# Kernel optimization log

Hardware: AMD Instinct MI355X
Metric: run time of the kernel (lower is better)

Reference implementation:

```python
import jax, jax.numpy as jnp
import numpy as np

OUT_STEPS = 32
UNITS = 512
FEATURES = 64


def setup_inputs() -> dict:
    key = jax.random.key(0)
    ks = jax.random.split(key, 4)
    B, T, F, U = 2048, 128, FEATURES, UNITS
    scale = 0.05
    return {
        "inputs": jax.random.normal(ks[0], (B, T, F), dtype=jnp.float32),
        "W_x": jax.random.normal(ks[1], (F, 4 * U), dtype=jnp.float32) * scale,
        "W_h": jax.random.normal(ks[2], (U, 4 * U), dtype=jnp.float32) * scale,
        "b": jnp.zeros((4 * U,), dtype=jnp.float32),
        "dense_W": jax.random.normal(ks[3], (U, F), dtype=jnp.float32) * scale,
        "dense_b": jnp.zeros((F,), dtype=jnp.float32),
    }


def reference(inputs, W_x, W_h, b, dense_W, dense_b):
    U = W_h.shape[0]
    B = inputs.shape[0]

    def cell(h, c, x):
        # Keras LSTMCell: gates in i, f, g(c), o order
        z = x @ W_x + h @ W_h + b  # [B, 4U]
        i, f, g, o = jnp.split(z, 4, axis=-1)
        i = jax.nn.sigmoid(i)
        f = jax.nn.sigmoid(f)
        g = jnp.tanh(g)
        o = jax.nn.sigmoid(o)
        c2 = f * c + i * g
        h2 = o * jnp.tanh(c2)
        return h2, c2

    h0 = jnp.zeros((B, U), inputs.dtype)
    c0 = jnp.zeros((B, U), inputs.dtype)

    def warm_step(carry, x_t):
        h, c = carry
        h, c = cell(h, c, x_t)
        return (h, c), None

    (h, c), _ = jax.lax.scan(warm_step, (h0, c0), jnp.swapaxes(inputs, 0, 1))
    pred = h @ dense_W + dense_b  # [B, F]

    def dec_step(carry, _):
        p, hh, cc = carry
        hh, cc = cell(hh, cc, p)
        p2 = hh @ dense_W + dense_b
        return (p2, hh, cc), p2

    _, rest = jax.lax.scan(dec_step, (pred, h, c), None, length=OUT_STEPS - 1)
    preds = jnp.concatenate([pred[None], rest], axis=0)  # [out_steps, B, F]
    return jnp.swapaxes(preds, 0, 1)  # [B, out_steps, F]
```

## Files before the change

### kernel.cpp

```cpp
#include <hip/hip_runtime.h>
#include <hip/hip_bf16.h>

#define B_ 2048
#define T_ 128
#define F_ 64
#define U_ 512
#define FOURU 2048
#define OUTS 32
#define ROWS 128
#define COLSB 128
#define KTOT 576
#define LDSTR 584

typedef __attribute__((ext_vector_type(8))) short bf16x8;
typedef __attribute__((ext_vector_type(4))) float f32x4;

#define OFF_CNT   0
#define OFF_HBUF  69632
#define OFF_WT    (OFF_HBUF + 2*B_*U_*2)
#define OFF_WDEC  (OFF_WT + FOURU*KTOT*2)
#define OFF_DWT   (OFF_WDEC + FOURU*U_*2)
#define OFF_BDEC  (OFF_DWT + F_*U_*2)
#define OFF_XBF   (OFF_BDEC + FOURU*4)
#define WS_TOTAL  (OFF_XBF + (size_t)T_*B_*F_*2)

__device__ __forceinline__ short f2bf(float f) {
  union { float f; unsigned u; } a; a.f = f;
  unsigned u = a.u;
  unsigned r = u + 0x7FFFu + ((u >> 16) & 1u);
  return (short)(r >> 16);
}
__device__ __forceinline__ float sigm(float x){ return 1.0f/(1.0f+__expf(-x)); }
__device__ __forceinline__ float tanh_(float x){ return 1.0f - 2.0f/(1.0f+__expf(2.0f*x)); }

__global__ void prep_wt(const float* __restrict__ Wx, const float* __restrict__ Wh,
                        short* __restrict__ Wt) {
  int idx = blockIdx.x*256 + threadIdx.x;
  if (idx >= FOURU*KTOT) return;
  int c = idx / KTOT, k = idx % KTOT;
  float v = (k < F_) ? Wx[(size_t)k*FOURU + c] : Wh[(size_t)(k-F_)*FOURU + c];
  Wt[idx] = f2bf(v);
}
__global__ void prep_wdec(const float* __restrict__ Wh, const float* __restrict__ Wx,
                          const float* __restrict__ Dw, short* __restrict__ Wdec) {
  int idx = blockIdx.x*256 + threadIdx.x;
  if (idx >= FOURU*U_) return;
  int c = idx / U_, u = idx % U_;
  float a = Wh[(size_t)u*FOURU + c];
  for (int f=0; f<F_; ++f) a += Dw[u*F_ + f] * Wx[(size_t)f*FOURU + c];
  Wdec[idx] = f2bf(a);
}
__global__ void prep_bdec(const float* __restrict__ bv, const float* __restrict__ db,
                          const float* __restrict__ Wx, float* __restrict__ bdec) {
  int c = blockIdx.x*256 + threadIdx.x;
  if (c >= FOURU) return;
  float a = bv[c];
  for (int f=0; f<F_; ++f) a += db[f]*Wx[(size_t)f*FOURU + c];
  bdec[c] = a;
}
__global__ void prep_dwt(const float* __restrict__ Dw, short* __restrict__ Dwt) {
  int idx = blockIdx.x*256 + threadIdx.x;
  if (idx >= F_*U_) return;
  int f = idx / U_, u = idx % U_;
  Dwt[idx] = f2bf(Dw[u*F_ + f]);
}
__global__ void prep_x(const float* __restrict__ in, short* __restrict__ xbf) {
  int idx = blockIdx.x*256 + threadIdx.x;
  if (idx >= T_*B_*F_) return;
  int f = idx % F_, b = (idx / F_) % B_, t = idx / (F_*B_);
  xbf[idx] = f2bf(in[((size_t)b*T_ + t)*F_ + f]);
}

__global__ __launch_bounds__(1024, 4) void lstm_main(
    const short* __restrict__ xbf, const short* __restrict__ Wt,
    const short* __restrict__ Wdec, const short* __restrict__ Dwt,
    const float* __restrict__ bvec, const float* __restrict__ bdec,
    const float* __restrict__ dbv, short* hbuf, unsigned* cnt,
    float* __restrict__ out)
{
  __shared__ short wlds[COLSB*LDSTR];
  __shared__ int sSame;
  const int tid = threadIdx.x;
  const int bidx = blockIdx.x;
  const int gb = (bidx & 7)*2 + (bidx >> 7);
  const int gu = (bidx >> 3) & 15;

  unsigned* flags  = cnt + gb*1024;
  unsigned* myFlag = flags + gu*64;
  unsigned* regCnt = cnt + 16384 + gb*16;
  unsigned* xcdTab = cnt + 16640 + gb*16;

  {
    unsigned xcc;
    asm volatile("s_getreg_b32 %0, hwreg(HW_REG_XCC_ID)" : "=s"(xcc));
    if (tid == 0) {
      __hip_atomic_store(&xcdTab[gu], xcc + 1u, __ATOMIC_RELAXED, __HIP_MEMORY_SCOPE_AGENT);
      __hip_atomic_fetch_add(regCnt, 1u, __ATOMIC_RELEASE, __HIP_MEMORY_SCOPE_AGENT);
      while (__hip_atomic_fetch_add(regCnt, 0u, __ATOMIC_RELAXED, __HIP_MEMORY_SCOPE_AGENT) < 16u)
        __builtin_amdgcn_s_sleep(2);
      __builtin_amdgcn_fence(__ATOMIC_ACQUIRE, "agent");
      unsigned x0 = __hip_atomic_load(&xcdTab[0], __ATOMIC_RELAXED, __HIP_MEMORY_SCOPE_AGENT);
      int same = 1;
      for (int i = 1; i < 16; ++i)
        same &= (__hip_atomic_load(&xcdTab[i], __ATOMIC_RELAXED, __HIP_MEMORY_SCOPE_AGENT) == x0);
      sSame = same;
    }
  }

  {
    const int c = tid >> 3, q = tid & 7;
    const int gate = (c >> 4) & 3;
    const int u = gu*32 + ((c >> 6) << 4) + (c & 15);
    const int gcol = gate*512 + u;
    const short* src = Wt + (size_t)gcol*KTOT + q*72;
    short* dst = wlds + c*LDSTR + q*72;
    #pragma unroll
    for (int j=0;j<9;j++)
      *(bf16x8*)(dst + j*8) = *(const bf16x8*)(src + j*8);
  }
  __syncthreads();
  const bool fastSync = (sSame != 0);

  const int w = tid >> 6, lane = tid & 63;
  const int wm = w >> 1, wn = w & 1;
  const int l15 = lane & 15, kh = lane >> 4;

  const int ucol = gu*32 + wn*16 + l15;
  float bia[4], biaD[4];
  #pragma unroll
  for (int g=0; g<4; ++g){ bia[g] = bvec[g*512 + ucol]; biaD[g] = bdec[g*512 + ucol]; }

  float cst[4] = {};
  const int rowA = gb*ROWS + wm*16 + l15;

  bf16x8 Bc[2][4];
  auto loadBc = [&]() {
    #pragma unroll
    for (int ks=0; ks<2; ++ks)
      #pragma unroll
      for (int g=0; g<4; ++g)
        Bc[ks][g] = *(const bf16x8*)(wlds + (size_t)(wn*64 + 16*g + l15)*LDSTR + 64 + ks*32 + kh*8);
  };
  loadBc();

  f32x4 acc[4];
  auto do_x = [&](int tt) {
    const short* xp = xbf + ((size_t)tt*B_ + rowA)*F_ + kh*8;
    bf16x8 a0 = *(const bf16x8*)(xp);
    bf16x8 a1 = *(const bf16x8*)(xp + 32);
    #pragma unroll
    for (int g=0; g<4; ++g) {
      bf16x8 b0 = *(const bf16x8*)(wlds + (size_t)(wn*64 + 16*g + l15)*LDSTR + kh*8);
      bf16x8 b1 = *(const bf16x8*)(wlds + (size_t)(wn*64 + 16*g + l15)*LDSTR + 32 + kh*8);
      f32x4 z = {0.f,0.f,0.f,0.f};
      z = __builtin_amdgcn_mfma_f32_16x16x32_bf16(a0, b0, z, 0,0,0);
      acc[g] = __builtin_amdgcn_mfma_f32_16x16x32_bf16(a1, b1, z, 0,0,0);
    }
  };
  do_x(0);

  for (int t = 0; t < 160; ++t) {
    if (t > 0) {
      if (fastSync) {
        if (tid < 64) {
          unsigned* fl = flags + (tid & 15)*64;
          const bool poller = (tid < 16);
          for (;;) {
            unsigned vv = poller
              ? __hip_atomic_load(fl, __ATOMIC_RELAXED, __HIP_MEMORY_SCOPE_AGENT)
              : (unsigned)t;
            if (__ballot(vv >= (unsigned)t) == ~0ull) break;
            __builtin_amdgcn_s_sleep(2);
          }
          asm volatile("buffer_inv sc0" ::: "memory");
          asm volatile("s_waitcnt vmcnt(0)" ::: "memory");
        }
      } else {
        if (tid < 64) {
          unsigned* fl = flags + (tid & 15)*64;
          const bool poller = (tid < 16);
          for (;;) {
            unsigned vv = poller
              ? __hip_atomic_fetch_add(fl, 0u, __ATOMIC_RELAXED, __HIP_MEMORY_SCOPE_AGENT)
              : (unsigned)t;
            if (__ballot(vv >= (unsigned)t) == ~0ull) break;
            __builtin_amdgcn_s_sleep(2);
          }
        }
        if (tid == 0)
          __builtin_amdgcn_fence(__ATOMIC_ACQUIRE, "agent");
      }
      __syncthreads();
    }

    const short* hcur = hbuf + (size_t)(t & 1)*B_*U_;
    short* hnxt = hbuf + (size_t)((t+1) & 1)*B_*U_;

    if (t >= 128 && gu < 8 && w < 4) {
      const int s = t - 128;
      const int pr0 = gb*ROWS + gu*16 + l15;
      f32x4 pa = {0.f,0.f,0.f,0.f};
      #pragma unroll
      for (int ks=0; ks<16; ++ks) {
        bf16x8 a = *(const bf16x8*)(hcur + (size_t)pr0*U_ + ks*32 + kh*8);
        bf16x8 b = *(const bf16x8*)(Dwt + (size_t)(w*16 + l15)*U_ + ks*32 + kh*8);
        pa = __builtin_amdgcn_mfma_f32_16x16x32_bf16(a, b, pa, 0,0,0);
      }
      const int col = w*16 + l15;
      const float dbc = dbv[col];
      #pragma unroll
      for (int r=0; r<4; ++r) {
        const int orow = gb*ROWS + gu*16 + kh*4 + r;
        out[((size_t)orow*OUTS + s)*F_ + col] = pa[r] + dbc;
      }
    }
    if (t == 159) break;
    if (t == 128) {
      __syncthreads();
      const int c = tid >> 3, q = tid & 7;
      const int gate = (c >> 4) & 3;
      const int u = gu*32 + ((c >> 6) << 4) + (c & 15);
      const int gcol = gate*512 + u;
      const short* src = Wdec + (size_t)gcol*U_ + q*64;
      short* dst = wlds + c*LDSTR + 64 + q*64;
      #pragma unroll
      for (int j=0;j<8;j++)
        *(bf16x8*)(dst + j*8) = *(const bf16x8*)(src + j*8);
      __syncthreads();
      loadBc();
    }

    {
      const short* hp = hcur + (size_t)rowA*U_ + kh*8;
      #pragma unroll
      for (int ks=0; ks<16; ++ks) {
        bf16x8 a = *(const bf16x8*)(hp + ks*32);
        #pragma unroll
        for (int g=0; g<4; ++g) {
          bf16x8 b = (ks < 2) ? Bc[ks][g]
            : *(const bf16x8*)(wlds + (size_t)(wn*64 + 16*g + l15)*LDSTR + 64 + ks*32 + kh*8);
          acc[g] = __builtin_amdgcn_mfma_f32_16x16x32_bf16(a, b, acc[g], 0,0,0);
        }
      }
    }

    {
      const bool warm = (t < T_);
      #pragma unroll
      for (int r=0; r<4; ++r) {
        float zi = acc[0][r] + (warm ? bia[0] : biaD[0]);
        float zf = acc[1][r] + (warm ? bia[1] : biaD[1]);
        float zg = acc[2][r] + (warm ? bia[2] : biaD[2]);
        float zo = acc[3][r] + (warm ? bia[3] : biaD[3]);
        float ig = sigm(zi), fg = sigm(zf), gg = tanh_(zg), og = sigm(zo);
        float c2 = fmaf(fg, cst[r], ig*gg);
        cst[r] = c2;
        float h2 = og*tanh_(c2);
        const int row = gb*ROWS + wm*16 + kh*4 + r;
        hnxt[(size_t)row*U_ + ucol] = f2bf(h2);
      }
    }

    __syncthreads();
    if (tid == 0) {
      if (fastSync)
        __hip_atomic_store(myFlag, (unsigned)(t+1), __ATOMIC_RELAXED, __HIP_MEMORY_SCOPE_AGENT);
      else
        __hip_atomic_fetch_add(myFlag, 1u, __ATOMIC_RELEASE, __HIP_MEMORY_SCOPE_AGENT);
    }

    #pragma unroll
    for (int g=0; g<4; ++g) acc[g] = (f32x4){0.f,0.f,0.f,0.f};
    if (t + 1 < T_) do_x(t+1);
  }
}

extern "C" void kernel_launch(void* const* d_in, const int* in_sizes, int n_in,
                              void* d_out, int out_size, void* d_ws, size_t ws_size,
                              hipStream_t stream) {
  const float* inputs = (const float*)d_in[0];
  const float* Wx = (const float*)d_in[1];
  const float* Wh = (const float*)d_in[2];
  const float* bv = (const float*)d_in[3];
  const float* Dw = (const float*)d_in[4];
  const float* db = (const float*)d_in[5];
  float* out = (float*)d_out;
  char* ws = (char*)d_ws;
  if (ws_size < WS_TOTAL) return;

  unsigned* cnt = (unsigned*)(ws + OFF_CNT);
  short* hbuf = (short*)(ws + OFF_HBUF);
  short* Wt   = (short*)(ws + OFF_WT);
  short* Wdec = (short*)(ws + OFF_WDEC);
  short* Dwt  = (short*)(ws + OFF_DWT);
  float* bdec = (float*)(ws + OFF_BDEC);
  short* xbf  = (short*)(ws + OFF_XBF);

  hipMemsetAsync(d_ws, 0, OFF_HBUF + (size_t)B_*U_*2, stream);
  prep_wt  <<<(FOURU*KTOT+255)/256, 256, 0, stream>>>(Wx, Wh, Wt);
  prep_wdec<<<(FOURU*U_ +255)/256, 256, 0, stream>>>(Wh, Wx, Dw, Wdec);
  prep_bdec<<<(FOURU     +255)/256, 256, 0, stream>>>(bv, db, Wx, bdec);
  prep_dwt <<<(F_*U_     +255)/256, 256, 0, stream>>>(Dw, Dwt);
  prep_x   <<<(T_*B_*F_  +255)/256, 256, 0, stream>>>(inputs, xbf);
  lstm_main<<<256, 1024, 0, stream>>>(xbf, Wt, Wdec, Dwt, bv, bdec, db, hbuf, cnt, out);
}
```

Before: 1.851 ms.

## Replace block-level barrier sync with per-wave flag counting and move dense head after publish

Each wave now polls the inter-block flags itself and bumps a shared counter after its own h stores. This replaces the block-wide __syncthreads and single-thread flag write, so waves no longer wait on the slowest wave in their block at each timestep. The dense output projection moves after the flag publish and is spread over the last two waves of every block instead of four waves in eight blocks. This takes it off the recurrence critical path. The register-cached B fragments are dropped, which frees registers but adds LDS reads, and the counter target now assumes 16 waves per block.

```diff
diff --git a/kernel.cpp b/kernel.cpp
--- a/kernel.cpp
+++ b/kernel.cpp
@@ -133,15 +133,8 @@
   float cst[4] = {};
   const int rowA = gb*ROWS + wm*16 + l15;
 
-  bf16x8 Bc[2][4];
-  auto loadBc = [&]() {
-    #pragma unroll
-    for (int ks=0; ks<2; ++ks)
-      #pragma unroll
-      for (int g=0; g<4; ++g)
-        Bc[ks][g] = *(const bf16x8*)(wlds + (size_t)(wn*64 + 16*g + l15)*LDSTR + 64 + ks*32 + kh*8);
-  };
-  loadBc();
+  const int predT  = gu*2 + (w - 14);
+  const int predRt = predT >> 2, predCt = predT & 3;
 
   f32x4 acc[4];
   auto do_x = [&](int tt) {
@@ -161,60 +154,36 @@
 
   for (int t = 0; t < 160; ++t) {
     if (t > 0) {
+      const unsigned target = 16u*(unsigned)t;
       if (fastSync) {
-        if (tid < 64) {
-          unsigned* fl = flags + (tid & 15)*64;
-          const bool poller = (tid < 16);
-          for (;;) {
-            unsigned vv = poller
-              ? __hip_atomic_load(fl, __ATOMIC_RELAXED, __HIP_MEMORY_SCOPE_AGENT)
-              : (unsigned)t;
-            if (__ballot(vv >= (unsigned)t) == ~0ull) break;
-            __builtin_amdgcn_s_sleep(2);
-          }
-          asm volatile("buffer_inv sc0" ::: "memory");
-          asm volatile("s_waitcnt vmcnt(0)" ::: "memory");
-        }
+        unsigned* fl = flags + (lane & 15)*64;
+        const bool poller = (lane < 16);
+        for (;;) {
+          unsigned vv = poller
+            ? __hip_atomic_load(fl, __ATOMIC_RELAXED, __HIP_MEMORY_SCOPE_AGENT)
+            : target;
+          if (__ballot(vv >= target) == ~0ull) break;
+          __builtin_amdgcn_s_sleep(1);
+        }
+        asm volatile("buffer_inv sc0" ::: "memory");
+        asm volatile("s_waitcnt vmcnt(0)" ::: "memory");
       } else {
-        if (tid < 64) {
-          unsigned* fl = flags + (tid & 15)*64;
-          const bool poller = (tid < 16);
-          for (;;) {
-            unsigned vv = poller
-              ? __hip_atomic_fetch_add(fl, 0u, __ATOMIC_RELAXED, __HIP_MEMORY_SCOPE_AGENT)
-              : (unsigned)t;
-            if (__ballot(vv >= (unsigned)t) == ~0ull) break;
-            __builtin_amdgcn_s_sleep(2);
-          }
-        }
-        if (tid == 0)
-          __builtin_amdgcn_fence(__ATOMIC_ACQUIRE, "agent");
-      }
-      __syncthreads();
+        unsigned* fl = flags + (lane & 15)*64;
+        const bool poller = (lane < 16);
+        for (;;) {
+          unsigned vv = poller
+            ? __hip_atomic_fetch_add(fl, 0u, __ATOMIC_RELAXED, __HIP_MEMORY_SCOPE_AGENT)
+            : target;
+          if (__ballot(vv >= target) == ~0ull) break;
+          __builtin_amdgcn_s_sleep(1);
+        }
+        __builtin_amdgcn_fence(__ATOMIC_ACQUIRE, "agent");
+      }
     }
 
     const short* hcur = hbuf + (size_t)(t & 1)*B_*U_;
     short* hnxt = hbuf + (size_t)((t+1) & 1)*B_*U_;
 
-    if (t >= 128 && gu < 8 && w < 4) {
-      const int s = t - 128;
-      const int pr0 = gb*ROWS + gu*16 + l15;
-      f32x4 pa = {0.f,0.f,0.f,0.f};
-      #pragma unroll
-      for (int ks=0; ks<16; ++ks) {
-        bf16x8 a = *(const bf16x8*)(hcur + (size_t)pr0*U_ + ks*32 + kh*8);
-        bf16x8 b = *(const bf16x8*)(Dwt + (size_t)(w*16 + l15)*U_ + ks*32 + kh*8);
-        pa = __builtin_amdgcn_mfma_f32_16x16x32_bf16(a, b, pa, 0,0,0);
-      }
-      const int col = w*16 + l15;
-      const float dbc = dbv[col];
-      #pragma unroll
-      for (int r=0; r<4; ++r) {
-        const int orow = gb*ROWS + gu*16 + kh*4 + r;
-        out[((size_t)orow*OUTS + s)*F_ + col] = pa[r] + dbc;
-      }
-    }
-    if (t == 159) break;
     if (t == 128) {
       __syncthreads();
       const int c = tid >> 3, q = tid & 7;
@@ -227,47 +196,67 @@
       for (int j=0;j<8;j++)
         *(bf16x8*)(dst + j*8) = *(const bf16x8*)(src + j*8);
       __syncthreads();
-      loadBc();
-    }
-
-    {
-      const short* hp = hcur + (size_t)rowA*U_ + kh*8;
+    }
+
+    if (t < 159) {
+      {
+        const short* hp = hcur + (size_t)rowA*U_ + kh*8;
+        #pragma unroll
+        for (int ks=0; ks<16; ++ks) {
+          bf16x8 a = *(const bf16x8*)(hp + ks*32);
+          #pragma unroll
+          for (int g=0; g<4; ++g) {
+            bf16x8 b = *(const bf16x8*)(wlds + (size_t)(wn*64 + 16*g + l15)*LDSTR + 64 + ks*32 + kh*8);
+            acc[g] = __builtin_amdgcn_mfma_f32_16x16x32_bf16(a, b, acc[g], 0,0,0);
+          }
+        }
+      }
+
+      {
+        const bool warm = (t < T_);
+        #pragma unroll
+        for (int r=0; r<4; ++r) {
+          float zi = acc[0][r] + (warm ? bia[0] : biaD[0]);
+          float zf = acc[1][r] + (warm ? bia[1] : biaD[1]);
+          float zg = acc[2][r] + (warm ? bia[2] : biaD[2]);
+          float zo = acc[3][r] + (warm ? bia[3] : biaD[3]);
+          float ig = sigm(zi), fg = sigm(zf), gg = tanh_(zg), og = sigm(zo);
+          float c2 = fmaf(fg, cst[r], ig*gg);
+          cst[r] = c2;
+          float h2 = og*tanh_(c2);
+          const int row = gb*ROWS + wm*16 + kh*4 + r;
+          hnxt[(size_t)row*U_ + ucol] = f2bf(h2);
+        }
+      }
+
+      asm volatile("s_waitcnt vmcnt(0)" ::: "memory");
+      if (lane == 0) {
+        if (fastSync)
+          __hip_atomic_fetch_add(myFlag, 1u, __ATOMIC_RELAXED, __HIP_MEMORY_SCOPE_AGENT);
+        else
+          __hip_atomic_fetch_add(myFlag, 1u, __ATOMIC_RELEASE, __HIP_MEMORY_SCOPE_AGENT);
+      }
+    }
+
+    if (t >= 128 && w >= 14) {
+      const int s = t - 128;
+      const int pr0 = gb*ROWS + predRt*16 + l15;
+      f32x4 pa = {0.f,0.f,0.f,0.f};
       #pragma unroll
       for (int ks=0; ks<16; ++ks) {
-        bf16x8 a = *(const bf16x8*)(hp + ks*32);
-        #pragma unroll
-        for (int g=0; g<4; ++g) {
-          bf16x8 b = (ks < 2) ? Bc[ks][g]
-            : *(const bf16x8*)(wlds + (size_t)(wn*64 + 16*g + l15)*LDSTR + 64 + ks*32 + kh*8);
-          acc[g] = __builtin_amdgcn_mfma_f32_16x16x32_bf16(a, b, acc[g], 0,0,0);
-        }
-      }
-    }
-
-    {
-      const bool warm = (t < T_);
+        bf16x8 a = *(const bf16x8*)(hcur + (size_t)pr0*U_ + ks*32 + kh*8);
+        bf16x8 b = *(const bf16x8*)(Dwt + (size_t)(predCt*16 + l15)*U_ + ks*32 + kh*8);
+        pa = __builtin_amdgcn_mfma_f32_16x16x32_bf16(a, b, pa, 0,0,0);
+      }
+      const int col = predCt*16 + l15;
+      const float dbc = dbv[col];
       #pragma unroll
       for (int r=0; r<4; ++r) {
-        float zi = acc[0][r] + (warm ? bia[0] : biaD[0]);
-        float zf = acc[1][r] + (warm ? bia[1] : biaD[1]);
-        float zg = acc[2][r] + (warm ? bia[2] : biaD[2]);
-        float zo = acc[3][r] + (warm ? bia[3] : biaD[3]);
-        float ig = sigm(zi), fg = sigm(zf), gg = tanh_(zg), og = sigm(zo);
-        float c2 = fmaf(fg, cst[r], ig*gg);
-        cst[r] = c2;
-        float h2 = og*tanh_(c2);
-        const int row = gb*ROWS + wm*16 + kh*4 + r;
-        hnxt[(size_t)row*U_ + ucol] = f2bf(h2);
-      }
-    }
-
-    __syncthreads();
-    if (tid == 0) {
-      if (fastSync)
-        __hip_atomic_store(myFlag, (unsigned)(t+1), __ATOMIC_RELAXED, __HIP_MEMORY_SCOPE_AGENT);
-      else
-        __hip_atomic_fetch_add(myFlag, 1u, __ATOMIC_RELEASE, __HIP_MEMORY_SCOPE_AGENT);
-    }
+        const int orow = gb*ROWS + predRt*16 + kh*4 + r;
+        out[((size_t)orow*OUTS + s)*F_ + col] = pa[r] + dbc;
+      }
+    }
+    if (t == 159) break;
 
     #pragma unroll
     for (int g=0; g<4; ++g) acc[g] = (f32x4){0.f,0.f,0.f,0.f};
```

After: 2.491 ms. +34.6%, slower.
